# Kernel optimization log

Measured on AMD Instinct MI355X. Metric: run time of the kernel, lower is better.

## Reference

```python
import jax, jax.numpy as jnp
import numpy as np

FP8_MAX = 448.0  # e4m3fn max representable magnitude


def _fp8_round(t):
    # round-trip through float8_e4m3fn emulates fp8 quantization rounding
    return t.astype(jnp.float8_e4m3fn).astype(t.dtype)


def setup_inputs() -> dict:
    key = jax.random.key(0)
    kx, kw, kb, ks = jax.random.split(key, 4)
    B, S, IN, OUT = 4, 2048, 4096, 4096
    x = jax.random.normal(kx, (B, S, IN), dtype=jnp.float16)
    # build an fp8-quantized weight exactly as the torch module does
    w = jax.random.uniform(kw, (OUT, IN), dtype=jnp.float16)
    w_s = (jnp.max(jnp.abs(w)).astype(jnp.float32) / FP8_MAX).reshape(1)
    w_fp8 = ((w.astype(jnp.float32) / w_s)
             .astype(jnp.float8_e4m3fn)
             .astype(jnp.float16))
    bias = jax.random.uniform(kb, (OUT,), dtype=jnp.float16)
    input_scale = jnp.ones((1,), dtype=jnp.float32)
    return {"x": x, "weight_fp8": w_fp8, "bias": bias,
            "input_scale": input_scale, "weight_scale": w_s}


def reference(x, weight_fp8, bias, input_scale, weight_scale):
    in_s = input_scale[0]
    w_s = weight_scale[0]
    # fake-quantize input to fp8 (per-tensor scale, clamp to e4m3 range)
    xq = jnp.clip(x.astype(jnp.float32) / in_s, -FP8_MAX, FP8_MAX)
    x_dq = _fp8_round(xq) * in_s                      # [B,S,IN] f32
    # dequantize fp8 weight
    w_dq = weight_fp8.astype(jnp.float32) * w_s       # [OUT,IN] f32
    out = jnp.einsum('bsi,oi->bso', x_dq, w_dq) + bias.astype(jnp.float32)
    return out.astype(x.dtype)
```

## Files before the change

kernel.cpp:

```cpp
#include <hip/hip_runtime.h>
#include <stdint.h>

typedef float  f32x4  __attribute__((ext_vector_type(4)));
typedef float  float4v __attribute__((ext_vector_type(4)));
typedef int    i32x4  __attribute__((ext_vector_type(4)));
typedef int    i32x8  __attribute__((ext_vector_type(8)));
typedef unsigned int u32x4 __attribute__((ext_vector_type(4)));

#define BM 128
#define BN 256
#define BKB 128

__device__ __forceinline__ unsigned f32_to_e4m3_sw(float t) {
    unsigned u = __float_as_uint(t);
    unsigned s = (u >> 24) & 0x80u;
    float ax = fabsf(t);
    if (ax < 0.015625f) {
        int m = (int)rintf(ax * 512.0f);
        return s | (unsigned)m;
    }
    unsigned au = u & 0x7fffffffu;
    unsigned r = au + 0x7FFFFu + ((au >> 20) & 1u);
    return s | (((r >> 23) - 120u) << 3) | ((r >> 20) & 7u);
}

__device__ __forceinline__ unsigned pack4_e4m3(float a, float b, float c, float d) {
#if __has_builtin(__builtin_amdgcn_cvt_pk_fp8_f32)
    int v = 0;
    v = __builtin_amdgcn_cvt_pk_fp8_f32(a, b, v, false);
    v = __builtin_amdgcn_cvt_pk_fp8_f32(c, d, v, true);
    return (unsigned)v;
#else
    return f32_to_e4m3_sw(a) | (f32_to_e4m3_sw(b) << 8) |
           (f32_to_e4m3_sw(c) << 16) | (f32_to_e4m3_sw(d) << 24);
#endif
}

__global__ void quant_kernel(const float4v* __restrict__ x, u32x4* __restrict__ xout, long nx16,
                             const float4v* __restrict__ w, u32x4* __restrict__ wout, long nw16,
                             const float* __restrict__ in_scale) {
    const float inv = 1.0f / in_scale[0];
    const long stride = (long)gridDim.x * blockDim.x;
    long i0 = (long)blockIdx.x * blockDim.x + threadIdx.x;
    for (long i = i0; i < nx16; i += stride) {
        u32x4 q;
#pragma unroll
        for (int j = 0; j < 4; ++j) {
            float4v v = x[i * 4 + j];
            float t0 = fminf(fmaxf(v[0] * inv, -448.0f), 448.0f);
            float t1 = fminf(fmaxf(v[1] * inv, -448.0f), 448.0f);
            float t2 = fminf(fmaxf(v[2] * inv, -448.0f), 448.0f);
            float t3 = fminf(fmaxf(v[3] * inv, -448.0f), 448.0f);
            q[j] = pack4_e4m3(t0, t1, t2, t3);
        }
        xout[i] = q;
    }
    for (long i = i0; i < nw16; i += stride) {
        u32x4 q;
#pragma unroll
        for (int j = 0; j < 4; ++j) {
            float4v v = w[i * 4 + j];
            q[j] = pack4_e4m3(v[0], v[1], v[2], v[3]);
        }
        wout[i] = q;
    }
}


__global__ __launch_bounds__(256, 2) void gemm_kernel(
    const unsigned char* __restrict__ A,
    const unsigned char* __restrict__ W,
    const float* __restrict__ bias,
    const float* __restrict__ in_scale,
    const float* __restrict__ w_scale,
    float* __restrict__ C, int M, int N, int K)
{
    __shared__ __align__(16) unsigned char sA[BM * BKB];
    __shared__ __align__(16) unsigned char sB[BN * BKB];

    const int tid  = threadIdx.x;
    const int wave = tid >> 6;
    const int lane = tid & 63;
    const int wr   = wave >> 1;
    const int wc   = wave & 1;

    const int nwg = gridDim.x;
    int bid = blockIdx.x, wgid;
    if ((nwg & 7) == 0) { const int cpx = nwg >> 3; wgid = (bid & 7) * cpx + (bid >> 3); }
    else wgid = bid;
    const int ntn  = N / BN;
    const int brow = (wgid / ntn) * BM;
    const int bcol = (wgid % ntn) * BN;

    const int rowInChunk = lane >> 3;
    const int pPhys      = (lane & 7) ^ rowInChunk;
    const int slotSrc    = 2 * (pPhys & 3) + (pPhys >> 2);

    f32x4 acc[4][8];
#pragma unroll
    for (int i = 0; i < 4; ++i)
#pragma unroll
        for (int j = 0; j < 8; ++j) { f32x4 z = {0.f,0.f,0.f,0.f}; acc[i][j] = z; }

    const int g = lane >> 4;

    for (int kt = 0; kt < K; kt += BKB) {
        if (kt) __syncthreads();
#pragma unroll
        for (int c = 0; c < 4; ++c) {
            const int chunk = wave * 4 + c;
            const int row   = chunk * 8 + rowInChunk;
            const unsigned char* ga = A + (long)(brow + row) * K + kt + slotSrc * 16;
            __builtin_amdgcn_global_load_lds(
                (const __attribute__((address_space(1))) unsigned int*)ga,
                (__attribute__((address_space(3))) unsigned int*)(sA + chunk * 1024), 16, 0, 0);
        }
#pragma unroll
        for (int c = 0; c < 8; ++c) {
            const int chunk = wave * 8 + c;
            const int row   = chunk * 8 + rowInChunk;
            const unsigned char* gb = W + (long)(bcol + row) * K + kt + slotSrc * 16;
            __builtin_amdgcn_global_load_lds(
                (const __attribute__((address_space(1))) unsigned int*)gb,
                (__attribute__((address_space(3))) unsigned int*)(sB + chunk * 1024), 16, 0, 0);
        }
        __syncthreads();

        i32x8 af[4];
#pragma unroll
        for (int mi = 0; mi < 4; ++mi) {
            const int row = wr * 64 + mi * 16 + (lane & 15);
            const int sl  = g ^ (row & 7);
            i32x4 lo = *(const i32x4*)(sA + row * 128 + sl * 16);
            i32x4 hi = *(const i32x4*)(sA + row * 128 + (sl ^ 4) * 16);
            i32x8 t;
            t[0]=lo[0]; t[1]=lo[1]; t[2]=lo[2]; t[3]=lo[3];
            t[4]=hi[0]; t[5]=hi[1]; t[6]=hi[2]; t[7]=hi[3];
            af[mi] = t;
        }
#pragma unroll
        for (int ni = 0; ni < 8; ++ni) {
            const int row = wc * 128 + ni * 16 + (lane & 15);
            const int sl  = g ^ (row & 7);
            i32x4 lo = *(const i32x4*)(sB + row * 128 + sl * 16);
            i32x4 hi = *(const i32x4*)(sB + row * 128 + (sl ^ 4) * 16);
            i32x8 bf;
            bf[0]=lo[0]; bf[1]=lo[1]; bf[2]=lo[2]; bf[3]=lo[3];
            bf[4]=hi[0]; bf[5]=hi[1]; bf[6]=hi[2]; bf[7]=hi[3];
#pragma unroll
            for (int mi = 0; mi < 4; ++mi)
                acc[mi][ni] = __builtin_amdgcn_mfma_scale_f32_16x16x128_f8f6f4(
                    af[mi], bf, acc[mi][ni],
                    0, 0, 0, 0x7F7F7F7F, 0, 0x7F7F7F7F);
        }
    }

    const float sc = in_scale[0] * w_scale[0];
#pragma unroll
    for (int ni = 0; ni < 8; ++ni) {
        const int n   = bcol + wc * 128 + ni * 16 + (lane & 15);
        const float bv = bias[n];
#pragma unroll
        for (int mi = 0; mi < 4; ++mi) {
            const int m0 = brow + wr * 64 + mi * 16 + ((lane >> 4) << 2);
#pragma unroll
            for (int r = 0; r < 4; ++r)
                C[(long)(m0 + r) * N + n] = fmaf(acc[mi][ni][r], sc, bv);
        }
    }
}

extern "C" void kernel_launch(void* const* d_in, const int* in_sizes, int n_in,
                              void* d_out, int out_size, void* d_ws, size_t ws_size,
                              hipStream_t stream) {
    const float* x    = (const float*)d_in[0];
    const float* w    = (const float*)d_in[1];
    const float* bias = (const float*)d_in[2];
    const float* in_s = (const float*)d_in[3];
    const float* w_s  = (const float*)d_in[4];
    float* out = (float*)d_out;

    const int  N   = in_sizes[2];
    const long wsz = (long)in_sizes[1];
    const int  K   = (int)(wsz / N);
    const long xsz = (long)in_sizes[0];
    const int  M   = (int)(xsz / K);

    unsigned char* xq = (unsigned char*)d_ws;
    unsigned char* wq = xq + (size_t)M * K;

    quant_kernel<<<2048, 256, 0, stream>>>((const float4v*)x, (u32x4*)xq, xsz / 16,
                                           (const float4v*)w, (u32x4*)wq, wsz / 16, in_s);

    dim3 grid((M / BM) * (N / BN));
    gemm_kernel<<<grid, 256, 0, stream>>>(xq, wq, bias, in_s, w_s, out, M, N, K);
}
```

Baseline: 170.6 us.

## Double-buffer the weight tile in LDS and prefetch the next K-step

The GEMM now keeps two LDS buffers for the B (weight) tile. It issues the global-to-LDS loads for the next K-step's B tile before computing the current one, and uses explicit vmcnt waits plus raw s_barrier so only the current A and B loads are waited on. This hides part of the global-load latency behind MFMA work. The cost is extra LDS (about 80KB per block), which may limit occupancy. The A tile is still loaded synchronously each step.

```diff
diff --git a/kernel.cpp b/kernel.cpp
--- a/kernel.cpp
+++ b/kernel.cpp
@@ -76,7 +76,7 @@
     float* __restrict__ C, int M, int N, int K)
 {
     __shared__ __align__(16) unsigned char sA[BM * BKB];
-    __shared__ __align__(16) unsigned char sB[BN * BKB];
+    __shared__ __align__(16) unsigned char sB[2][BN * BKB];
 
     const int tid  = threadIdx.x;
     const int wave = tid >> 6;
@@ -104,27 +104,48 @@
 
     const int g = lane >> 4;
 
-    for (int kt = 0; kt < K; kt += BKB) {
-        if (kt) __syncthreads();
-#pragma unroll
-        for (int c = 0; c < 4; ++c) {
-            const int chunk = wave * 4 + c;
-            const int row   = chunk * 8 + rowInChunk;
-            const unsigned char* ga = A + (long)(brow + row) * K + kt + slotSrc * 16;
-            __builtin_amdgcn_global_load_lds(
-                (const __attribute__((address_space(1))) unsigned int*)ga,
-                (__attribute__((address_space(3))) unsigned int*)(sA + chunk * 1024), 16, 0, 0);
-        }
-#pragma unroll
-        for (int c = 0; c < 8; ++c) {
-            const int chunk = wave * 8 + c;
-            const int row   = chunk * 8 + rowInChunk;
-            const unsigned char* gb = W + (long)(bcol + row) * K + kt + slotSrc * 16;
-            __builtin_amdgcn_global_load_lds(
-                (const __attribute__((address_space(1))) unsigned int*)gb,
-                (__attribute__((address_space(3))) unsigned int*)(sB + chunk * 1024), 16, 0, 0);
-        }
-        __syncthreads();
+    const int NT = K / BKB;
+
+#define STAGE_A(kt)                                                               \
+    {                                                                             \
+        _Pragma("unroll")                                                         \
+        for (int c = 0; c < 4; ++c) {                                             \
+            const int chunk = wave * 4 + c;                                       \
+            const int row   = chunk * 8 + rowInChunk;                             \
+            const unsigned char* ga = A + (long)(brow + row) * K + (kt) + slotSrc * 16; \
+            __builtin_amdgcn_global_load_lds(                                     \
+                (const __attribute__((address_space(1))) unsigned int*)ga,        \
+                (__attribute__((address_space(3))) unsigned int*)(sA + chunk * 1024), 16, 0, 0); \
+        }                                                                         \
+    }
+
+#define STAGE_B(bi, kt)                                                           \
+    {                                                                             \
+        _Pragma("unroll")                                                         \
+        for (int c = 0; c < 8; ++c) {                                             \
+            const int chunk = wave * 8 + c;                                       \
+            const int row   = chunk * 8 + rowInChunk;                             \
+            const unsigned char* gb = W + (long)(bcol + row) * K + (kt) + slotSrc * 16; \
+            __builtin_amdgcn_global_load_lds(                                     \
+                (const __attribute__((address_space(1))) unsigned int*)gb,        \
+                (__attribute__((address_space(3))) unsigned int*)(sB[bi] + chunk * 1024), 16, 0, 0); \
+        }                                                                         \
+    }
+
+    STAGE_B(0, 0);
+
+    for (int t = 0; t < NT; ++t) {
+        const int b = t & 1;
+        if (t) __builtin_amdgcn_s_barrier();
+
+        STAGE_A(t * BKB);
+        if (t + 1 < NT) {
+            STAGE_B(b ^ 1, (t + 1) * BKB);
+            asm volatile("s_waitcnt vmcnt(8)" ::: "memory");
+        } else {
+            asm volatile("s_waitcnt vmcnt(0)" ::: "memory");
+        }
+        __builtin_amdgcn_s_barrier();
 
         i32x8 af[4];
 #pragma unroll
@@ -133,17 +154,17 @@
             const int sl  = g ^ (row & 7);
             i32x4 lo = *(const i32x4*)(sA + row * 128 + sl * 16);
             i32x4 hi = *(const i32x4*)(sA + row * 128 + (sl ^ 4) * 16);
-            i32x8 t;
-            t[0]=lo[0]; t[1]=lo[1]; t[2]=lo[2]; t[3]=lo[3];
-            t[4]=hi[0]; t[5]=hi[1]; t[6]=hi[2]; t[7]=hi[3];
-            af[mi] = t;
+            i32x8 tv;
+            tv[0]=lo[0]; tv[1]=lo[1]; tv[2]=lo[2]; tv[3]=lo[3];
+            tv[4]=hi[0]; tv[5]=hi[1]; tv[6]=hi[2]; tv[7]=hi[3];
+            af[mi] = tv;
         }
 #pragma unroll
         for (int ni = 0; ni < 8; ++ni) {
             const int row = wc * 128 + ni * 16 + (lane & 15);
             const int sl  = g ^ (row & 7);
-            i32x4 lo = *(const i32x4*)(sB + row * 128 + sl * 16);
-            i32x4 hi = *(const i32x4*)(sB + row * 128 + (sl ^ 4) * 16);
+            i32x4 lo = *(const i32x4*)(sB[b] + row * 128 + sl * 16);
+            i32x4 hi = *(const i32x4*)(sB[b] + row * 128 + (sl ^ 4) * 16);
             i32x8 bf;
             bf[0]=lo[0]; bf[1]=lo[1]; bf[2]=lo[2]; bf[3]=lo[3];
             bf[4]=hi[0]; bf[5]=hi[1]; bf[6]=hi[2]; bf[7]=hi[3];
@@ -154,6 +175,8 @@
                     0, 0, 0, 0x7F7F7F7F, 0, 0x7F7F7F7F);
         }
     }
+#undef STAGE_A
+#undef STAGE_B
 
     const float sc = in_scale[0] * w_scale[0];
 #pragma unroll
```

Result: no change. 173.3 us (+1.6%).
